# Kernel optimization log

Measured on AMD Instinct MI355X. Metric: run time of the kernel, lower is better.

## Reference

```python
import jax, jax.numpy as jnp
import numpy as np

N_NODES = 50000
N_EDGES = 640000
HID = 128
LN_EPS = 1e-5


def setup_inputs() -> dict:
    key = jax.random.key(0)
    ks = jax.random.split(key, 8)
    x = jax.random.normal(ks[0], (N_NODES, HID), dtype=jnp.float32)
    edge_index = jax.random.randint(ks[1], (2, N_EDGES), 0, N_NODES, dtype=jnp.int64)
    edge_attr = jax.random.normal(ks[2], (N_EDGES, HID), dtype=jnp.float32)
    # parameters (Kaiming-ish scaling)
    msg_W1 = jax.random.normal(ks[3], (3 * HID, HID), dtype=jnp.float32) / np.sqrt(3 * HID)
    msg_b1 = jnp.zeros((HID,), dtype=jnp.float32)
    msg_W2 = jax.random.normal(ks[4], (HID, HID), dtype=jnp.float32) / np.sqrt(HID)
    msg_b2 = jnp.zeros((HID,), dtype=jnp.float32)
    upd_W1 = jax.random.normal(ks[5], (2 * HID, HID), dtype=jnp.float32) / np.sqrt(2 * HID)
    upd_b1 = jnp.zeros((HID,), dtype=jnp.float32)
    upd_W2 = jax.random.normal(ks[6], (HID, HID), dtype=jnp.float32) / np.sqrt(HID)
    upd_b2 = jnp.zeros((HID,), dtype=jnp.float32)
    ln_gamma = jnp.ones((HID,), dtype=jnp.float32)
    ln_beta = jnp.zeros((HID,), dtype=jnp.float32)
    return {
        'x': x, 'edge_index': edge_index, 'edge_attr': edge_attr,
        'msg_W1': msg_W1, 'msg_b1': msg_b1, 'msg_W2': msg_W2, 'msg_b2': msg_b2,
        'upd_W1': upd_W1, 'upd_b1': upd_b1, 'upd_W2': upd_W2, 'upd_b2': upd_b2,
        'ln_gamma': ln_gamma, 'ln_beta': ln_beta,
    }


def _layer_norm(h, gamma, beta):
    mu = jnp.mean(h, axis=-1, keepdims=True)
    var = jnp.mean(jnp.square(h - mu), axis=-1, keepdims=True)
    return (h - mu) * jax.lax.rsqrt(var + LN_EPS) * gamma + beta


def reference(x, edge_index, edge_attr,
              msg_W1, msg_b1, msg_W2, msg_b2,
              upd_W1, upd_b1, upd_W2, upd_b2,
              ln_gamma, ln_beta):
    src, dst = edge_index[0], edge_index[1]
    # batched per-edge gather + concat: [E, 3*HID]
    msg_in = jnp.concatenate([x[src], x[dst], edge_attr], axis=-1)
    # message MLP (dropout is identity in eval)
    h = jax.nn.relu(msg_in @ msg_W1 + msg_b1)
    messages = h @ msg_W2 + msg_b2  # [E, HID]
    # scatter-add aggregation by destination node
    aggregated = jax.ops.segment_sum(messages, dst, num_segments=x.shape[0])
    # update MLP
    upd_in = jnp.concatenate([x, aggregated], axis=-1)  # [N, 2*HID]
    u = jax.nn.relu(upd_in @ upd_W1 + upd_b1)
    updated = u @ upd_W2 + upd_b2
    return _layer_norm(x + updated, ln_gamma, ln_beta)
```

## Files before the change

kernel.cpp:

```cpp
#include <hip/hip_runtime.h>

#define HID 128

typedef __attribute__((ext_vector_type(8))) short short8;
typedef __attribute__((ext_vector_type(4))) float f32x4;

__device__ __forceinline__ float bf2f(unsigned short u) {
  union { unsigned int u; float f; } c; c.u = ((unsigned int)u) << 16; return c.f;
}
__device__ __forceinline__ unsigned short f2bf(float f) {
  union { float f; unsigned int u; } c; c.f = f;
  unsigned int u = c.u;
  return (unsigned short)((u + 0x7FFFu + ((u >> 16) & 1u)) >> 16);
}
__device__ __forceinline__ float loads(const void* p, size_t i, bool f32) {
  return f32 ? ((const float*)p)[i] : bf2f(((const unsigned short*)p)[i]);
}
__device__ __forceinline__ short8 load_a8(const void* base, size_t row, int k, bool f32) {
  if (!f32) return *(const short8*)((const unsigned short*)base + row * HID + k);
  const float* fp = (const float*)base + row * HID + k;
  f32x4 f0 = *(const f32x4*)fp;
  f32x4 f1 = *(const f32x4*)(fp + 4);
  short8 t;
  t[0] = (short)f2bf(f0[0]); t[1] = (short)f2bf(f0[1]);
  t[2] = (short)f2bf(f0[2]); t[3] = (short)f2bf(f0[3]);
  t[4] = (short)f2bf(f1[0]); t[5] = (short)f2bf(f1[1]);
  t[6] = (short)f2bf(f1[2]); t[7] = (short)f2bf(f1[3]);
  return t;
}

__global__ void detect_kernel(const void* __restrict__ x,
                              const int* __restrict__ eidx,
                              int* __restrict__ flags) {
  __shared__ int bad, oddnz;
  if (threadIdx.x == 0) { bad = 0; oddnz = 0; }
  __syncthreads();
  const unsigned short* xu = (const unsigned short*)x;
  int mybad = 0;
  for (int i = threadIdx.x; i < 4096; i += 256) {
    int ef = (xu[i] >> 7) & 0xFF;
    if (!(ef == 0 || (ef >= 90 && ef <= 140))) mybad++;
  }
  if (mybad) atomicAdd(&bad, mybad);
  int t = threadIdx.x;
  if (t < 128) {
    if (eidx[2 * t + 1] != 0) atomicAdd(&oddnz, 1);
  }
  __syncthreads();
  if (threadIdx.x == 0) {
    flags[0] = (bad > 409) ? 1 : 0;
    flags[1] = (oddnz == 0) ? 1 : 0;
  }
}

__global__ void zero_out_kernel(unsigned int* __restrict__ out,
                                const int* __restrict__ flags, long long nelem) {
  bool f32 = flags[0] != 0;
  size_t words = (size_t)nelem * (f32 ? 2 : 1) / 2;
  for (size_t w = blockIdx.x * 256ull + threadIdx.x; w < words; w += (size_t)gridDim.x * 256ull)
    out[w] = 0u;
}

__global__ void repack_all(const void* __restrict__ W1, const void* __restrict__ W2,
                           const void* __restrict__ U1, const void* __restrict__ U2,
                           unsigned short* __restrict__ P1, unsigned short* __restrict__ P2,
                           unsigned short* __restrict__ PU1, unsigned short* __restrict__ PU2,
                           const int* __restrict__ flags) {
  const bool f32 = flags[0] != 0;
  int idx = blockIdx.x * 256 + threadIdx.x;
  const int s1 = 384 * 128, s2 = s1 + 128 * 128, s3 = s2 + 256 * 128, s4 = s3 + 128 * 128;
  if (idx >= s4) return;
  const void* W; unsigned short* P; int off;
  if (idx < s1)      { W = W1; P = P1;  off = idx; }
  else if (idx < s2) { W = W2; P = P2;  off = idx - s1; }
  else if (idx < s3) { W = U1; P = PU1; off = idx - s2; }
  else               { W = U2; P = PU2; off = idx - s3; }
  int j = off & 7, lane = (off >> 3) & 63, ct = (off >> 9) & 7, ks = off >> 12;
  int k = ks * 32 + ((lane >> 4) << 3) + j;
  int n = ct * 16 + (lane & 15);
  P[off] = f2bf(loads(W, (size_t)k * 128 + n, f32));
}

__global__ __launch_bounds__(256) void edge_kernel(
    const void* __restrict__ x, const int* __restrict__ eidx,
    const void* __restrict__ eattr,
    const unsigned short* __restrict__ P1, const void* __restrict__ b1,
    const unsigned short* __restrict__ P2, const void* __restrict__ b2,
    float* __restrict__ aggf, void* __restrict__ out,
    const int* __restrict__ flags, int E, int N, int small_mode) {
  __shared__ unsigned short hs[64][136];
  const bool f32 = flags[0] != 0;
  const bool i64 = flags[1] != 0;
  const int tid  = threadIdx.x;
  const int lane = tid & 63;
  const int wid  = tid >> 6;
  const int l15  = lane & 15;
  const int quad = lane >> 4;
  const int base = blockIdx.x * 64;

  int me = base + wid * 16 + l15;
  if (me >= E) me = E - 1;
  int src = i64 ? eidx[2 * me] : eidx[me];
  int dsm = i64 ? eidx[2 * (E + me)] : eidx[E + me];
  src = min(max(src, 0), N - 1);
  dsm = min(max(dsm, 0), N - 1);

  f32x4 zero = {0.f, 0.f, 0.f, 0.f};
  f32x4 acc[8];
#pragma unroll
  for (int ct = 0; ct < 8; ct++) acc[ct] = zero;

#pragma unroll
  for (int ks = 0; ks < 12; ks++) {
    const int k0 = ks * 32;
    short8 a;
    if (k0 < 128)      a = load_a8(x,     (size_t)src, k0 + quad * 8, f32);
    else if (k0 < 256) a = load_a8(x,     (size_t)dsm, (k0 - 128) + quad * 8, f32);
    else               a = load_a8(eattr, (size_t)me,  (k0 - 256) + quad * 8, f32);
    const unsigned short* wp = P1 + ((size_t)(ks * 8) * 64 + lane) * 8;
#pragma unroll
    for (int ct = 0; ct < 8; ct++) {
      short8 b = *(const short8*)(wp + ct * 512);
      acc[ct] = __builtin_amdgcn_mfma_f32_16x16x32_bf16(a, b, acc[ct], 0, 0, 0);
    }
  }

#pragma unroll
  for (int ct = 0; ct < 8; ct++) {
    const int col = ct * 16 + l15;
    const float bv = loads(b1, col, f32);
#pragma unroll
    for (int r = 0; r < 4; r++) {
      float v = acc[ct][r] + bv;
      hs[wid * 16 + quad * 4 + r][col] = f2bf(fmaxf(v, 0.f));
    }
  }
  __syncthreads();

  f32x4 acc2[8];
#pragma unroll
  for (int ct = 0; ct < 8; ct++) acc2[ct] = zero;
#pragma unroll
  for (int ks = 0; ks < 4; ks++) {
    short8 a = *(const short8*)&hs[wid * 16 + l15][ks * 32 + quad * 8];
    const unsigned short* wp = P2 + ((size_t)(ks * 8) * 64 + lane) * 8;
#pragma unroll
    for (int ct = 0; ct < 8; ct++) {
      short8 b = *(const short8*)(wp + ct * 512);
      acc2[ct] = __builtin_amdgcn_mfma_f32_16x16x32_bf16(a, b, acc2[ct], 0, 0, 0);
    }
  }

  float b2v[8];
#pragma unroll
  for (int ct = 0; ct < 8; ct++) b2v[ct] = loads(b2, ct * 16 + l15, f32);

  if (!small_mode || f32) {
    float* tgt = (!small_mode) ? aggf : (float*)out;
#pragma unroll
    for (int r = 0; r < 4; r++) {
      const int e = base + wid * 16 + quad * 4 + r;
      if (e < E) {
        int d = i64 ? eidx[2 * (E + e)] : eidx[E + e];
        d = min(max(d, 0), N - 1);
        float* op = tgt + (size_t)d * HID + l15;
#pragma unroll
        for (int ct = 0; ct < 8; ct++) atomicAdd(op + ct * 16, acc2[ct][r] + b2v[ct]);
      }
    }
  } else {
#pragma unroll
    for (int ct = 0; ct < 8; ct++) {
      const int col = ct * 16 + l15;
#pragma unroll
      for (int r = 0; r < 4; r++)
        hs[wid * 16 + quad * 4 + r][col] = f2bf(acc2[ct][r] + b2v[ct]);
    }
    __syncthreads();
    const int row = tid >> 2;
    const int cg  = (tid & 3) * 32;
    const int e = base + row;
    if (e < E) {
      int d = i64 ? eidx[2 * (E + e)] : eidx[E + e];
      d = min(max(d, 0), N - 1);
      unsigned int* orow = (unsigned int*)out + ((size_t)d * HID >> 1);
#pragma unroll
      for (int p = 0; p < 16; p++) {
        const int col = cg + p * 2;
        const float lo = bf2f(hs[row][col]);
        const float hi = bf2f(hs[row][col + 1]);
        unsigned int* wp = orow + (col >> 1);
        unsigned int old = *wp, assumed;
        do {
          assumed = old;
          unsigned int nv = (unsigned int)f2bf(bf2f((unsigned short)(assumed & 0xFFFF)) + lo)
                          | ((unsigned int)f2bf(bf2f((unsigned short)(assumed >> 16)) + hi) << 16);
          old = atomicCAS(wp, assumed, nv);
        } while (old != assumed);
      }
    }
  }
}

__global__ __launch_bounds__(256) void node_kernel(
    const void* __restrict__ x, const float* __restrict__ aggf,
    const unsigned short* __restrict__ PU1, const void* __restrict__ ub1,
    const unsigned short* __restrict__ PU2, const void* __restrict__ ub2,
    const void* __restrict__ gamma, const void* __restrict__ beta,
    void* __restrict__ out, const int* __restrict__ flags, int N, int small_mode) {
  __shared__ unsigned short hs[64][136];
  const bool f32 = flags[0] != 0;
  const int tid  = threadIdx.x;
  const int lane = tid & 63;
  const int wid  = tid >> 6;
  const int l15  = lane & 15;
  const int quad = lane >> 4;
  const int base = blockIdx.x * 64;

  int mn = base + wid * 16 + l15;
  if (mn >= N) mn = N - 1;

  const void* aggp = (!small_mode) ? (const void*)aggf : (const void*)out;
  const bool aggF32 = (!small_mode) ? true : f32;

  f32x4 zero = {0.f, 0.f, 0.f, 0.f};
  f32x4 acc[8];
#pragma unroll
  for (int ct = 0; ct < 8; ct++) acc[ct] = zero;

#pragma unroll
  for (int ks = 0; ks < 8; ks++) {
    const int k0 = ks * 32;
    short8 a;
    if (k0 < 128) a = load_a8(x,    (size_t)mn, k0 + quad * 8, f32);
    else          a = load_a8(aggp, (size_t)mn, (k0 - 128) + quad * 8, aggF32);
    const unsigned short* wp = PU1 + ((size_t)(ks * 8) * 64 + lane) * 8;
#pragma unroll
    for (int ct = 0; ct < 8; ct++) {
      short8 b = *(const short8*)(wp + ct * 512);
      acc[ct] = __builtin_amdgcn_mfma_f32_16x16x32_bf16(a, b, acc[ct], 0, 0, 0);
    }
  }

#pragma unroll
  for (int ct = 0; ct < 8; ct++) {
    const int col = ct * 16 + l15;
    const float bv = loads(ub1, col, f32);
#pragma unroll
    for (int r = 0; r < 4; r++) {
      float v = acc[ct][r] + bv;
      hs[wid * 16 + quad * 4 + r][col] = f2bf(fmaxf(v, 0.f));
    }
  }
  __syncthreads();

  f32x4 acc2[8];
#pragma unroll
  for (int ct = 0; ct < 8; ct++) acc2[ct] = zero;
#pragma unroll
  for (int ks = 0; ks < 4; ks++) {
    short8 a = *(const short8*)&hs[wid * 16 + l15][ks * 32 + quad * 8];
    const unsigned short* wp = PU2 + ((size_t)(ks * 8) * 64 + lane) * 8;
#pragma unroll
    for (int ct = 0; ct < 8; ct++) {
      short8 b = *(const short8*)(wp + ct * 512);
      acc2[ct] = __builtin_amdgcn_mfma_f32_16x16x32_bf16(a, b, acc2[ct], 0, 0, 0);
    }
  }

  float vals[8][4];
  float s1[4] = {0.f, 0.f, 0.f, 0.f};
  float s2[4] = {0.f, 0.f, 0.f, 0.f};
#pragma unroll
  for (int ct = 0; ct < 8; ct++) {
    const int col = ct * 16 + l15;
    const float bv = loads(ub2, col, f32);
#pragma unroll
    for (int r = 0; r < 4; r++) {
      int row = base + wid * 16 + quad * 4 + r;
      int rc = row < N ? row : 0;
      float v = acc2[ct][r] + bv + loads(x, (size_t)rc * HID + col, f32);
      vals[ct][r] = v;
      s1[r] += v;
      s2[r] += v * v;
    }
  }
#pragma unroll
  for (int off = 1; off < 16; off <<= 1) {
#pragma unroll
    for (int r = 0; r < 4; r++) {
      s1[r] += __shfl_xor(s1[r], off, 16);
      s2[r] += __shfl_xor(s2[r], off, 16);
    }
  }
#pragma unroll
  for (int r = 0; r < 4; r++) {
    const int row = base + wid * 16 + quad * 4 + r;
    if (row < N) {
      const float mean = s1[r] * (1.0f / 128.0f);
      const float var  = fmaxf(s2[r] * (1.0f / 128.0f) - mean * mean, 0.0f);
      const float rstd = rsqrtf(var + 1e-5f);
#pragma unroll
      for (int ct = 0; ct < 8; ct++) {
        const int col = ct * 16 + l15;
        float o = (vals[ct][r] - mean) * rstd * loads(gamma, col, f32) + loads(beta, col, f32);
        if (f32) ((float*)out)[(size_t)row * HID + col] = o;
        else     ((unsigned short*)out)[(size_t)row * HID + col] = f2bf(o);
      }
    }
  }
}

extern "C" void kernel_launch(void* const* d_in, const int* in_sizes, int n_in,
                              void* d_out, int out_size, void* d_ws, size_t ws_size,
                              hipStream_t stream) {
  (void)n_in;
  const void* x     = d_in[0];
  const int*  eidx  = (const int*)d_in[1];
  const void* eattr = d_in[2];
  const void* W1  = d_in[3];
  const void* b1  = d_in[4];
  const void* W2  = d_in[5];
  const void* b2  = d_in[6];
  const void* U1  = d_in[7];
  const void* ub1 = d_in[8];
  const void* U2  = d_in[9];
  const void* ub2 = d_in[10];
  const void* gam = d_in[11];
  const void* bet = d_in[12];

  const int N = in_sizes[0] / HID;
  const int E = in_sizes[2] / HID;

  char* ws = (char*)d_ws;
  int* flags = (int*)ws;
  unsigned short* P1  = (unsigned short*)(ws + 256);
  unsigned short* P2  = (unsigned short*)(ws + 256 + 98304);
  unsigned short* PU1 = (unsigned short*)(ws + 256 + 131072);
  unsigned short* PU2 = (unsigned short*)(ws + 256 + 196608);
  const size_t agg_off = 256 + 229376;
  float* aggf = (float*)(ws + agg_off);
  const size_t need = agg_off + (size_t)N * HID * sizeof(float);
  const int small_mode = (ws_size < need) ? 1 : 0;

  detect_kernel<<<1, 256, 0, stream>>>(x, eidx, flags);
  if (!small_mode) {
    hipMemsetAsync(aggf, 0, (size_t)N * HID * sizeof(float), stream);
  } else {
    zero_out_kernel<<<1024, 256, 0, stream>>>((unsigned int*)d_out, flags, (long long)out_size);
  }
  repack_all<<<448, 256, 0, stream>>>(W1, W2, U1, U2, P1, P2, PU1, PU2, flags);
  edge_kernel<<<(E + 63) / 64, 256, 0, stream>>>(x, eidx, eattr, P1, b1, P2, b2,
                                                 aggf, d_out, flags, E, N, small_mode);
  node_kernel<<<(N + 63) / 64, 256, 0, stream>>>(x, aggf, PU1, ub1, PU2, ub2,
                                                 gam, bet, d_out, flags, N, small_mode);
}
```

Baseline: 900.2 us.

## Sort edges by destination and pre-reduce messages before atomic scatter

Adds a counting sort of edges by destination node (histogram, single-block scan, scatter into sorted src/dst/perm arrays). The edge kernel then processes edges in sorted order, staging messages in shared memory and summing consecutive rows that share a destination before issuing atomics. This is meant to cut the number of global float atomics, which is one per edge per column in the plain path. The cost is extra kernels, including a serial single-block scan over all nodes, extra workspace, and gathers of edge_attr through the permutation. The old unsorted path is kept as a fallback when workspace is too small.

```diff
diff --git a/kernel.cpp b/kernel.cpp
--- a/kernel.cpp
+++ b/kernel.cpp
@@ -42,15 +42,21 @@
     if (!(ef == 0 || (ef >= 90 && ef <= 140))) mybad++;
   }
   if (mybad) atomicAdd(&bad, mybad);
-  int t = threadIdx.x;
-  if (t < 128) {
-    if (eidx[2 * t + 1] != 0) atomicAdd(&oddnz, 1);
+  if (threadIdx.x < 128) {
+    if (eidx[2 * threadIdx.x + 1] != 0) atomicAdd(&oddnz, 1);
   }
   __syncthreads();
   if (threadIdx.x == 0) {
     flags[0] = (bad > 409) ? 1 : 0;
     flags[1] = (oddnz == 0) ? 1 : 0;
   }
+}
+
+__device__ __forceinline__ int get_dst(const int* eidx, bool i64, int E, int e) {
+  return i64 ? eidx[2 * (E + e)] : eidx[E + e];
+}
+__device__ __forceinline__ int get_src(const int* eidx, bool i64, int E, int e) {
+  return i64 ? eidx[2 * e] : eidx[e];
 }
 
 __global__ void zero_out_kernel(unsigned int* __restrict__ out,
@@ -81,7 +87,173 @@
   P[off] = f2bf(loads(W, (size_t)k * 128 + n, f32));
 }
 
-__global__ __launch_bounds__(256) void edge_kernel(
+__global__ void hist_kernel(const int* __restrict__ eidx, int* __restrict__ counts,
+                            const int* __restrict__ flags, int E, int N) {
+  const bool i64 = flags[1] != 0;
+  int e = blockIdx.x * 256 + threadIdx.x;
+  if (e < E) {
+    int d = get_dst(eidx, i64, E, e);
+    d = min(max(d, 0), N - 1);
+    atomicAdd(&counts[d], 1);
+  }
+}
+
+__global__ __launch_bounds__(1024) void scan_kernel(const int* __restrict__ counts,
+                                                    int* __restrict__ offs, int N) {
+  __shared__ int wsum[16];
+  __shared__ int wpre[16];
+  __shared__ int carry_s;
+  const int tid = threadIdx.x, lane = tid & 63, wid = tid >> 6;
+  if (tid == 0) carry_s = 0;
+  __syncthreads();
+  for (int base = 0; base < N; base += 1024) {
+    int i = base + tid;
+    int v = (i < N) ? counts[i] : 0;
+    int s = v;
+#pragma unroll
+    for (int off = 1; off < 64; off <<= 1) {
+      int t = __shfl_up(s, off, 64);
+      if (lane >= off) s += t;
+    }
+    if (lane == 63) wsum[wid] = s;
+    __syncthreads();
+    if (tid == 0) {
+      int run = carry_s;
+#pragma unroll
+      for (int w = 0; w < 16; w++) { int t = wsum[w]; wpre[w] = run; run += t; }
+      carry_s = run;
+    }
+    __syncthreads();
+    if (i < N) offs[i] = wpre[wid] + s - v;
+    __syncthreads();
+  }
+  if (tid == 0) offs[N] = carry_s;
+}
+
+__global__ void scatter_kernel(const int* __restrict__ eidx, int* __restrict__ cur,
+                               int* __restrict__ ssrc, int* __restrict__ sdst,
+                               int* __restrict__ perm,
+                               const int* __restrict__ flags, int E, int N) {
+  const bool i64 = flags[1] != 0;
+  int e = blockIdx.x * 256 + threadIdx.x;
+  if (e < E) {
+    int d = get_dst(eidx, i64, E, e);
+    int s = get_src(eidx, i64, E, e);
+    d = min(max(d, 0), N - 1);
+    s = min(max(s, 0), N - 1);
+    int pos = atomicAdd(&cur[d], 1);
+    ssrc[pos] = s;
+    sdst[pos] = d;
+    perm[pos] = e;
+  }
+}
+
+__global__ __launch_bounds__(256) void edge_kernel_sorted(
+    const void* __restrict__ x, const void* __restrict__ eattr,
+    const int* __restrict__ ssrc, const int* __restrict__ sdst,
+    const int* __restrict__ perm,
+    const unsigned short* __restrict__ P1, const void* __restrict__ b1,
+    const unsigned short* __restrict__ P2, const void* __restrict__ b2,
+    float* __restrict__ aggf, const int* __restrict__ flags, int E, int N) {
+  __shared__ __align__(16) char smem[64 * 132 * 4];
+  __shared__ int sdst_s[64];
+  unsigned short (*hs)[136] = (unsigned short (*)[136])smem;
+  float (*ms)[132] = (float (*)[132])smem;
+  const bool f32 = flags[0] != 0;
+  const int tid  = threadIdx.x;
+  const int lane = tid & 63;
+  const int wid  = tid >> 6;
+  const int l15  = lane & 15;
+  const int quad = lane >> 4;
+  const int base = blockIdx.x * 64;
+
+  if (tid < 64) sdst_s[tid] = sdst[min(base + tid, E - 1)];
+
+  int me = base + wid * 16 + l15;
+  if (me >= E) me = E - 1;
+  const int src = ssrc[me];
+  const int dsm = sdst[me];
+  const int pe  = perm[me];
+
+  f32x4 zero = {0.f, 0.f, 0.f, 0.f};
+  f32x4 acc[8];
+#pragma unroll
+  for (int ct = 0; ct < 8; ct++) acc[ct] = zero;
+
+#pragma unroll
+  for (int ks = 0; ks < 12; ks++) {
+    const int k0 = ks * 32;
+    short8 a;
+    if (k0 < 128)      a = load_a8(x,     (size_t)src, k0 + quad * 8, f32);
+    else if (k0 < 256) a = load_a8(x,     (size_t)dsm, (k0 - 128) + quad * 8, f32);
+    else               a = load_a8(eattr, (size_t)pe,  (k0 - 256) + quad * 8, f32);
+    const unsigned short* wp = P1 + ((size_t)(ks * 8) * 64 + lane) * 8;
+#pragma unroll
+    for (int ct = 0; ct < 8; ct++) {
+      short8 b = *(const short8*)(wp + ct * 512);
+      acc[ct] = __builtin_amdgcn_mfma_f32_16x16x32_bf16(a, b, acc[ct], 0, 0, 0);
+    }
+  }
+
+#pragma unroll
+  for (int ct = 0; ct < 8; ct++) {
+    const int col = ct * 16 + l15;
+    const float bv = loads(b1, col, f32);
+#pragma unroll
+    for (int r = 0; r < 4; r++) {
+      float v = acc[ct][r] + bv;
+      hs[wid * 16 + quad * 4 + r][col] = f2bf(fmaxf(v, 0.f));
+    }
+  }
+
+  f32x4 acc2[8];
+#pragma unroll
+  for (int ct = 0; ct < 8; ct++) acc2[ct] = zero;
+#pragma unroll
+  for (int ks = 0; ks < 4; ks++) {
+    short8 a = *(const short8*)&hs[wid * 16 + l15][ks * 32 + quad * 8];
+    const unsigned short* wp = P2 + ((size_t)(ks * 8) * 64 + lane) * 8;
+#pragma unroll
+    for (int ct = 0; ct < 8; ct++) {
+      short8 b = *(const short8*)(wp + ct * 512);
+      acc2[ct] = __builtin_amdgcn_mfma_f32_16x16x32_bf16(a, b, acc2[ct], 0, 0, 0);
+    }
+  }
+
+  float b2v[8];
+#pragma unroll
+  for (int ct = 0; ct < 8; ct++) b2v[ct] = loads(b2, ct * 16 + l15, f32);
+
+  __syncthreads();
+#pragma unroll
+  for (int ct = 0; ct < 8; ct++) {
+    const int col = ct * 16 + l15;
+#pragma unroll
+    for (int r = 0; r < 4; r++) {
+      const int e = base + wid * 16 + quad * 4 + r;
+      ms[wid * 16 + quad * 4 + r][col] = (e < E) ? (acc2[ct][r] + b2v[ct]) : 0.0f;
+    }
+  }
+  __syncthreads();
+
+  const int col  = tid & 127;
+  const int half = tid >> 7;
+  const int r0 = half * 32;
+  float sum = 0.0f;
+  int cur = sdst_s[r0];
+#pragma unroll 4
+  for (int r = r0; r < r0 + 32; r++) {
+    int d = sdst_s[r];
+    if (d != cur) {
+      atomicAdd(&aggf[(size_t)cur * HID + col], sum);
+      sum = 0.0f; cur = d;
+    }
+    sum += ms[r][col];
+  }
+  atomicAdd(&aggf[(size_t)cur * HID + col], sum);
+}
+
+__global__ __launch_bounds__(256) void edge_kernel_plain(
     const void* __restrict__ x, const int* __restrict__ eidx,
     const void* __restrict__ eattr,
     const unsigned short* __restrict__ P1, const void* __restrict__ b1,
@@ -100,8 +272,8 @@
 
   int me = base + wid * 16 + l15;
   if (me >= E) me = E - 1;
-  int src = i64 ? eidx[2 * me] : eidx[me];
-  int dsm = i64 ? eidx[2 * (E + me)] : eidx[E + me];
+  int src = get_src(eidx, i64, E, me);
+  int dsm = get_dst(eidx, i64, E, me);
   src = min(max(src, 0), N - 1);
   dsm = min(max(dsm, 0), N - 1);
 
@@ -109,7 +281,6 @@
   f32x4 acc[8];
 #pragma unroll
   for (int ct = 0; ct < 8; ct++) acc[ct] = zero;
-
 #pragma unroll
   for (int ks = 0; ks < 12; ks++) {
     const int k0 = ks * 32;
@@ -124,19 +295,15 @@
       acc[ct] = __builtin_amdgcn_mfma_f32_16x16x32_bf16(a, b, acc[ct], 0, 0, 0);
     }
   }
-
 #pragma unroll
   for (int ct = 0; ct < 8; ct++) {
     const int col = ct * 16 + l15;
     const float bv = loads(b1, col, f32);
 #pragma unroll
-    for (int r = 0; r < 4; r++) {
-      float v = acc[ct][r] + bv;
-      hs[wid * 16 + quad * 4 + r][col] = f2bf(fmaxf(v, 0.f));
-    }
-  }
-  __syncthreads();
-
+    for (int r = 0; r < 4; r++)
+      hs[wid * 16 + quad * 4 + r][col] = f2bf(fmaxf(acc[ct][r] + bv, 0.f));
+  }
+  __syncthreads();
   f32x4 acc2[8];
 #pragma unroll
   for (int ct = 0; ct < 8; ct++) acc2[ct] = zero;
@@ -150,7 +317,6 @@
       acc2[ct] = __builtin_amdgcn_mfma_f32_16x16x32_bf16(a, b, acc2[ct], 0, 0, 0);
     }
   }
-
   float b2v[8];
 #pragma unroll
   for (int ct = 0; ct < 8; ct++) b2v[ct] = loads(b2, ct * 16 + l15, f32);
@@ -161,7 +327,7 @@
     for (int r = 0; r < 4; r++) {
       const int e = base + wid * 16 + quad * 4 + r;
       if (e < E) {
-        int d = i64 ? eidx[2 * (E + e)] : eidx[E + e];
+        int d = get_dst(eidx, i64, E, e);
         d = min(max(d, 0), N - 1);
         float* op = tgt + (size_t)d * HID + l15;
 #pragma unroll
@@ -181,7 +347,7 @@
     const int cg  = (tid & 3) * 32;
     const int e = base + row;
     if (e < E) {
-      int d = i64 ? eidx[2 * (E + e)] : eidx[E + e];
+      int d = get_dst(eidx, i64, E, e);
       d = min(max(d, 0), N - 1);
       unsigned int* orow = (unsigned int*)out + ((size_t)d * HID >> 1);
 #pragma unroll
@@ -227,7 +393,6 @@
   f32x4 acc[8];
 #pragma unroll
   for (int ct = 0; ct < 8; ct++) acc[ct] = zero;
-
 #pragma unroll
   for (int ks = 0; ks < 8; ks++) {
     const int k0 = ks * 32;
@@ -241,19 +406,15 @@
       acc[ct] = __builtin_amdgcn_mfma_f32_16x16x32_bf16(a, b, acc[ct], 0, 0, 0);
     }
   }
-
 #pragma unroll
   for (int ct = 0; ct < 8; ct++) {
     const int col = ct * 16 + l15;
     const float bv = loads(ub1, col, f32);
 #pragma unroll
-    for (int r = 0; r < 4; r++) {
-      float v = acc[ct][r] + bv;
-      hs[wid * 16 + quad * 4 + r][col] = f2bf(fmaxf(v, 0.f));
-    }
-  }
-  __syncthreads();
-
+    for (int r = 0; r < 4; r++)
+      hs[wid * 16 + quad * 4 + r][col] = f2bf(fmaxf(acc[ct][r] + bv, 0.f));
+  }
+  __syncthreads();
   f32x4 acc2[8];
 #pragma unroll
   for (int ct = 0; ct < 8; ct++) acc2[ct] = zero;
@@ -340,18 +501,52 @@
   unsigned short* PU2 = (unsigned short*)(ws + 256 + 196608);
   const size_t agg_off = 256 + 229376;
   float* aggf = (float*)(ws + agg_off);
-  const size_t need = agg_off + (size_t)N * HID * sizeof(float);
-  const int small_mode = (ws_size < need) ? 1 : 0;
+  const size_t agg_bytes = (size_t)N * HID * sizeof(float);
+
+  size_t o = agg_off + agg_bytes;
+  auto alignup = [](size_t v) { return (v + 255) & ~(size_t)255; };
+  o = alignup(o);           size_t offs_off = o; o += (size_t)(N + 1) * 4;
+  o = alignup(o);           size_t cur_off  = o; o += (size_t)(N + 1) * 4;
+  o = alignup(o);           size_t ssrc_off = o; o += (size_t)E * 4;
+  o = alignup(o);           size_t sdst_off = o; o += (size_t)E * 4;
+  o = alignup(o);           size_t perm_off = o; o += (size_t)E * 4;
+  const size_t need_sort  = o;
+  const size_t need_basic = agg_off + agg_bytes;
+
+  int* offsb = (int*)(ws + offs_off);
+  int* curb  = (int*)(ws + cur_off);
+  int* ssrc  = (int*)(ws + ssrc_off);
+  int* sdst  = (int*)(ws + sdst_off);
+  int* perm  = (int*)(ws + perm_off);
+
+  const int mode = (ws_size >= need_sort) ? 2 : ((ws_size >= need_basic) ? 1 : 0);
 
   detect_kernel<<<1, 256, 0, stream>>>(x, eidx, flags);
-  if (!small_mode) {
-    hipMemsetAsync(aggf, 0, (size_t)N * HID * sizeof(float), stream);
+  repack_all<<<448, 256, 0, stream>>>(W1, W2, U1, U2, P1, P2, PU1, PU2, flags);
+
+  if (mode == 2) {
+    hipMemsetAsync(aggf, 0, agg_bytes, stream);
+    hipMemsetAsync(curb, 0, (size_t)(N + 1) * 4, stream);
+    hist_kernel<<<(E + 255) / 256, 256, 0, stream>>>(eidx, curb, flags, E, N);
+    scan_kernel<<<1, 1024, 0, stream>>>(curb, offsb, N);
+    hipMemcpyAsync(curb, offsb, (size_t)(N + 1) * 4, hipMemcpyDeviceToDevice, stream);
+    scatter_kernel<<<(E + 255) / 256, 256, 0, stream>>>(eidx, curb, ssrc, sdst, perm,
+                                                        flags, E, N);
+    edge_kernel_sorted<<<(E + 63) / 64, 256, 0, stream>>>(x, eattr, ssrc, sdst, perm,
+                                                          P1, b1, P2, b2, aggf, flags, E, N);
+    node_kernel<<<(N + 63) / 64, 256, 0, stream>>>(x, aggf, PU1, ub1, PU2, ub2,
+                                                   gam, bet, d_out, flags, N, 0);
+  } else if (mode == 1) {
+    hipMemsetAsync(aggf, 0, agg_bytes, stream);
+    edge_kernel_plain<<<(E + 63) / 64, 256, 0, stream>>>(x, eidx, eattr, P1, b1, P2, b2,
+                                                         aggf, d_out, flags, E, N, 0);
+    node_kernel<<<(N + 63) / 64, 256, 0, stream>>>(x, aggf, PU1, ub1, PU2, ub2,
+                                                   gam, bet, d_out, flags, N, 0);
   } else {
     zero_out_kernel<<<1024, 256, 0, stream>>>((unsigned int*)d_out, flags, (long long)out_size);
-  }
-  repack_all<<<448, 256, 0, stream>>>(W1, W2, U1, U2, P1, P2, PU1, PU2, flags);
-  edge_kernel<<<(E + 63) / 64, 256, 0, stream>>>(x, eidx, eattr, P1, b1, P2, b2,
-                                                 aggf, d_out, flags, E, N, small_mode);
-  node_kernel<<<(N + 63) / 64, 256, 0, stream>>>(x, aggf, PU1, ub1, PU2, ub2,
-                                                 gam, bet, d_out, flags, N, small_mode);
-}
+    edge_kernel_plain<<<(E + 63) / 64, 256, 0, stream>>>(x, eidx, eattr, P1, b1, P2, b2,
+                                                         aggf, d_out, flags, E, N, 1);
+    node_kernel<<<(N + 63) / 64, 256, 0, stream>>>(x, aggf, PU1, ub1, PU2, ub2,
+                                                   gam, bet, d_out, flags, N, 1);
+  }
+}
```

Measured after the change: 903.0 us. No clear change (+0.3%).
